# Kernel optimization log

Measured on AMD Instinct MI355X. Metric: run time of the kernel, lower is better.

The kernel has to match this reference:

```python
import jax, jax.numpy as jnp
import numpy as np

N_HEADS = 8

def setup_inputs() -> dict:
    key = jax.random.key(0)
    ks = jax.random.split(key, 12)
    B, S2, C, H, W = 2, 2048, 1280, 256, 256
    s = 0.02  # weight init scale
    return {
        'hidden_states': jax.random.normal(ks[0], (B, S2, C), dtype=jnp.float32),
        'src_mask': (jax.random.uniform(ks[1], (B, 1, H, W)) > 0.5).astype(jnp.float32),
        'attn_wq': jax.random.normal(ks[2], (C, C), dtype=jnp.float32) * s,
        'attn_wk': jax.random.normal(ks[3], (C, C), dtype=jnp.float32) * s,
        'attn_wv': jax.random.normal(ks[4], (C, C), dtype=jnp.float32) * s,
        'out_w': jax.random.normal(ks[5], (C, C), dtype=jnp.float32) * s,
        'out_b': jnp.zeros((C,), dtype=jnp.float32),
        'proc_wq': jax.random.normal(ks[6], (C, C), dtype=jnp.float32) * s,
        'proc_wk': jax.random.normal(ks[7], (C, C), dtype=jnp.float32) * s,
        'proc_wv': jax.random.normal(ks[8], (C, C), dtype=jnp.float32) * s,
        'ww': jax.random.normal(ks[9], (C + 1, 1), dtype=jnp.float32) * s,
        'wb': jnp.zeros((1,), dtype=jnp.float32),
    }


def reference(hidden_states, src_mask, attn_wq, attn_wk, attn_wv, out_w, out_b,
              proc_wq, proc_wk, proc_wv, ww, wb):
    B, S2, C = hidden_states.shape
    S = S2 // 2  # condition_flag=False: sequence is two images concatenated
    _, _, H, W = src_mask.shape
    r = int(np.sqrt((H * W) / S))  # nearest-neighbor downsample ratio
    # F.interpolate(mode='nearest') with exact integer ratio == strided slice
    m = src_mask[:, 0, ::r, ::r].reshape(B, S, 1)          # [B, S, 1]
    mask = jnp.concatenate([m, m], axis=1)                 # [B, 2S, 1]
    # sigmoid gate blending the two query projections
    gate_in = jnp.concatenate([hidden_states, mask], axis=-1)  # [B, 2S, C+1]
    w = jax.nn.sigmoid(gate_in @ ww + wb)                  # [B, 2S, 1]
    query = (hidden_states @ attn_wq) * w + (hidden_states @ proc_wq) * (1.0 - w)
    # keys/values: first half through attn's projections, second half through processor's
    e1, e2 = hidden_states[:, :S], hidden_states[:, S:]
    key = jnp.concatenate([e1 @ attn_wk, e2 @ proc_wk], axis=1)
    value = jnp.concatenate([e1 @ attn_wv, e2 @ proc_wv], axis=1)
    d = C // N_HEADS
    def split_heads(x):
        return x.reshape(B, S2, N_HEADS, d).transpose(0, 2, 1, 3)  # [B, H, S2, d]
    qh, kh, vh = split_heads(query), split_heads(key), split_heads(value)
    scale = float(1.0 / np.sqrt(d))
    scores = jnp.einsum('bhqd,bhkd->bhqk', qh, kh) * scale
    probs = jax.nn.softmax(scores, axis=-1)
    out = jnp.einsum('bhqk,bhkd->bhqd', probs, vh)
    out = out.transpose(0, 2, 1, 3).reshape(B, S2, C)
    out = out @ out_w + out_b
    # residual connection, rescale_output_factor == 1
    return out + hidden_states
```

## Files before the change

### kernel.cpp

```cpp
#include <hip/hip_runtime.h>

typedef unsigned short u16;
typedef u16 u16x4 __attribute__((ext_vector_type(4)));
typedef u16 u16x8 __attribute__((ext_vector_type(8)));
typedef __bf16 bf16x8 __attribute__((ext_vector_type(8)));
typedef float f32x4 __attribute__((ext_vector_type(4)));
typedef unsigned u32x4 __attribute__((ext_vector_type(4)));

#define DEVI __device__ __forceinline__

#if __has_builtin(__builtin_amdgcn_exp2f)
#define EXP2F __builtin_amdgcn_exp2f
#else
#define EXP2F exp2f
#endif

DEVI u16 f2b(float f) {
  unsigned u = __builtin_bit_cast(unsigned, f);
  u += 0x7fffu + ((u >> 16) & 1u);
  return (u16)(u >> 16);
}

DEVI float b2f(u16 v) { return __builtin_bit_cast(float, (unsigned)v << 16); }

DEVI unsigned cvtpk_bf16(float lo, float hi) {
  unsigned r;
  asm("v_cvt_pk_bf16_f32 %0, %1, %2" : "=v"(r) : "v"(lo), "v"(hi));
  return r;
}

DEVI f32x4 mfma16(u16x8 a, u16x8 b, f32x4 c) {
  return __builtin_amdgcn_mfma_f32_16x16x32_bf16(
      __builtin_bit_cast(bf16x8, a), __builtin_bit_cast(bf16x8, b), c, 0, 0, 0);
}

DEVI void async_copy16(const u16* g, u16* l) {
  __builtin_amdgcn_global_load_lds(
      (__attribute__((address_space(1))) unsigned int*)(g),
      (__attribute__((address_space(3))) unsigned int*)(l), 16, 0, 0);
}

DEVI void fence_barrier() {
  asm volatile("" ::: "memory");
  __builtin_amdgcn_s_barrier();
  asm volatile("" ::: "memory");
}

__global__ void prep_kernel(const float* __restrict__ hs, const float* __restrict__ mask,
                            const float* __restrict__ ww, const float* __restrict__ wb,
                            u16* __restrict__ hsb, float* __restrict__ wgate) {
  int token = blockIdx.x;
  int tid = threadIdx.x;
  const float* row = hs + (size_t)token * 1280;
  u16* orow = hsb + (size_t)token * 1280;
  float acc = 0.f;
#pragma unroll
  for (int i = 0; i < 5; i++) {
    int c = i * 256 + tid;
    float v = row[c];
    orow[c] = f2b(v);
    acc += v * ww[c];
  }
#pragma unroll
  for (int off = 1; off < 64; off <<= 1) acc += __shfl_xor(acc, off);
  __shared__ float partial[4];
  int wid = tid >> 6;
  if ((tid & 63) == 0) partial[wid] = acc;
  __syncthreads();
  if (tid == 0) {
    float tot = partial[0] + partial[1] + partial[2] + partial[3];
    int b = token >> 11, t = token & 2047;
    int s = t & 1023;
    float mv = mask[b * 65536 + ((s >> 5) * 8) * 256 + (s & 31) * 8];
    float z = tot + mv * ww[1280] + wb[0];
    wgate[token] = 1.f / (1.f + __expf(-z));
  }
}

__global__ void wtrans_kernel(const float* w0, const float* w1, const float* w2,
                              const float* w3, const float* w4, const float* w5,
                              const float* w6, u16* __restrict__ out) {
  const float* src;
  switch (blockIdx.z) {
    case 0: src = w0; break; case 1: src = w1; break; case 2: src = w2; break;
    case 3: src = w3; break; case 4: src = w4; break; case 5: src = w5; break;
    default: src = w6; break;
  }
  u16* dst = out + (size_t)blockIdx.z * 1280 * 1280;
  __shared__ float tile[32][33];
  int tx = threadIdx.x & 31, ty = threadIdx.x >> 5;
  int k0 = blockIdx.x * 32, n0 = blockIdx.y * 32;
#pragma unroll
  for (int r = 0; r < 4; r++)
    tile[ty + r * 8][tx] = src[(size_t)(k0 + ty + r * 8) * 1280 + n0 + tx];
  __syncthreads();
#pragma unroll
  for (int r = 0; r < 4; r++)
    dst[(size_t)(n0 + ty + r * 8) * 1280 + k0 + tx] = f2b(tile[tx][ty + r * 8]);
}

__launch_bounds__(256, 4)
__global__ void gemm_qdual_kernel(const u16* __restrict__ A, const u16* __restrict__ Wt,
                                  const float* __restrict__ wgate, float qscale,
                                  u16* __restrict__ Qout) {
  const int K = 1280, N = 1280;
  const size_t WSZ = (size_t)1280 * 1280;
  __shared__ u16 As[2][128 * 32];
  __shared__ u16 Bs[2][64 * 32];
  __shared__ u16 Bs2[2][64 * 32];

  int tid = threadIdx.x;
  int wid = tid >> 6, lane = tid & 63;
  int q = lane & 15, jl = lane >> 4;
  int nb = blockIdx.x, mb = blockIdx.y, z = blockIdx.z;
  int m0 = mb * 128, n0 = nb * 128;

  const u16* B0 = Wt + 0 * WSZ;
  const u16* B1 = Wt + 4 * WSZ;

  f32x4 zero = {0.f, 0.f, 0.f, 0.f};
  f32x4 acc[4][4];
#pragma unroll
  for (int i = 0; i < 4; i++)
#pragma unroll
    for (int j = 0; j < 4; j++) acc[i][j] = zero;

  int wr = wid >> 1, wc = wid & 1;
  int brow = tid >> 2, bseg = tid & 3;
  int nrow = n0 + (z << 6) + brow;

#define QSTAGE(buf, kk)                                                           \
  do {                                                                            \
    int k0 = (kk) * 32;                                                           \
    _Pragma("unroll") for (int i = 0; i < 2; i++) {                               \
      int slot = i * 256 + tid;                                                   \
      int row = slot >> 2, seg = slot & 3;                                        \
      async_copy16(A + (size_t)(m0 + row) * K + k0 + seg * 8,                     \
                   As[buf] + (size_t)(i * 256 + wid * 64) * 8);                   \
    }                                                                             \
    async_copy16(B0 + (size_t)nrow * K + k0 + bseg * 8, Bs[buf] + (size_t)tid * 8);   \
    async_copy16(B1 + (size_t)nrow * K + k0 + bseg * 8, Bs2[buf] + (size_t)tid * 8);  \
  } while (0)

  QSTAGE(0, 0);
  for (int kk = 0; kk < 40; kk++) {
    int cur = kk & 1;
    if (kk < 39) {
      QSTAGE(cur ^ 1, kk + 1);
      asm volatile("s_waitcnt vmcnt(4)" ::: "memory");
    } else {
      asm volatile("s_waitcnt vmcnt(0)" ::: "memory");
    }
    fence_barrier();

    u16x8 af[4];
#pragma unroll
    for (int mi = 0; mi < 4; mi++)
      af[mi] = *(const u16x8*)(As[cur] + (wr * 64 + mi * 16 + q) * 32 + jl * 8);
#pragma unroll
    for (int ni = 0; ni < 2; ni++) {
      u16x8 bf0 = *(const u16x8*)(Bs[cur] + (wc * 32 + ni * 16 + q) * 32 + jl * 8);
      u16x8 bf1 = *(const u16x8*)(Bs2[cur] + (wc * 32 + ni * 16 + q) * 32 + jl * 8);
#pragma unroll
      for (int mi = 0; mi < 4; mi++) {
        acc[mi][ni] = mfma16(af[mi], bf0, acc[mi][ni]);
        acc[mi][2 + ni] = mfma16(af[mi], bf1, acc[mi][2 + ni]);
      }
    }
    fence_barrier();
  }
#undef QSTAGE

#pragma unroll
  for (int mi = 0; mi < 4; mi++)
#pragma unroll
    for (int r = 0; r < 4; r++) {
      int row = m0 + wr * 64 + mi * 16 + (jl << 2) + r;
      float w = wgate[row];
#pragma unroll
      for (int ni = 0; ni < 2; ni++) {
        int col = n0 + (z << 6) + wc * 32 + ni * 16 + q;
        float v = (w * acc[mi][ni][r] + (1.f - w) * acc[mi][2 + ni][r]) * qscale;
        Qout[(size_t)row * N + col] = f2b(v);
      }
    }
}

__launch_bounds__(256, 4)
__global__ void gemm_kv_kernel(const u16* __restrict__ A, const u16* __restrict__ Wt,
                               u16* __restrict__ Kout, u16* __restrict__ VTout) {
  const int K = 1280, N = 1280;
  const size_t WSZ = (size_t)1280 * 1280;
  __shared__ u16 As[2][128 * 32];
  __shared__ u16 Bs[2][64 * 32];
  __shared__ u16 Bs2[2][64 * 32];

  int tid = threadIdx.x;
  int wid = tid >> 6, lane = tid & 63;
  int q = lane & 15, jl = lane >> 4;
  int nb = blockIdx.x, mb = blockIdx.y;
  bool isV = (blockIdx.z == 1);
  int m0 = mb * 128, n0 = nb * 128;
  bool first = ((m0 & 2047) < 1024);

  const u16* B0 = isV ? (first ? Wt + 2 * WSZ : Wt + 6 * WSZ)
                      : (first ? Wt + 1 * WSZ : Wt + 5 * WSZ);

  f32x4 zero = {0.f, 0.f, 0.f, 0.f};
  f32x4 acc[4][4];
#pragma unroll
  for (int i = 0; i < 4; i++)
#pragma unroll
    for (int j = 0; j < 4; j++) acc[i][j] = zero;

  int wr = wid >> 1, wc = wid & 1;
  int brow = tid >> 2, bseg = tid & 3;

#define KVSTAGE(buf, kk)                                                          \
  do {                                                                            \
    int k0 = (kk) * 32;                                                           \
    _Pragma("unroll") for (int i = 0; i < 2; i++) {                               \
      int slot = i * 256 + tid;                                                   \
      int row = slot >> 2, seg = slot & 3;                                        \
      async_copy16(A + (size_t)(m0 + row) * K + k0 + seg * 8,                     \
                   As[buf] + (size_t)(i * 256 + wid * 64) * 8);                   \
    }                                                                             \
    async_copy16(B0 + (size_t)(n0 + brow) * K + k0 + bseg * 8, Bs[buf] + (size_t)tid * 8);       \
    async_copy16(B0 + (size_t)(n0 + 64 + brow) * K + k0 + bseg * 8, Bs2[buf] + (size_t)tid * 8); \
  } while (0)

  KVSTAGE(0, 0);
  for (int kk = 0; kk < 40; kk++) {
    int cur = kk & 1;
    if (kk < 39) {
      KVSTAGE(cur ^ 1, kk + 1);
      asm volatile("s_waitcnt vmcnt(4)" ::: "memory");
    } else {
      asm volatile("s_waitcnt vmcnt(0)" ::: "memory");
    }
    fence_barrier();

    u16x8 af[4];
#pragma unroll
    for (int mi = 0; mi < 4; mi++)
      af[mi] = *(const u16x8*)(As[cur] + (wr * 64 + mi * 16 + q) * 32 + jl * 8);
    const u16* Bsel = wc ? Bs2[cur] : Bs[cur];
    u16x8 bfr[4];
#pragma unroll
    for (int ni = 0; ni < 4; ni++)
      bfr[ni] = *(const u16x8*)(Bsel + (ni * 16 + q) * 32 + jl * 8);
#pragma unroll
    for (int mi = 0; mi < 4; mi++)
#pragma unroll
      for (int ni = 0; ni < 4; ni++)
        acc[mi][ni] = mfma16(af[mi], bfr[ni], acc[mi][ni]);
    fence_barrier();
  }
#undef KVSTAGE

  if (!isV) {
#pragma unroll
    for (int mi = 0; mi < 4; mi++)
#pragma unroll
      for (int ni = 0; ni < 4; ni++)
#pragma unroll
        for (int r = 0; r < 4; r++) {
          int row = m0 + wr * 64 + mi * 16 + (jl << 2) + r;
          int col = n0 + wc * 64 + ni * 16 + q;
          Kout[(size_t)row * N + col] = f2b(acc[mi][ni][r]);
        }
  } else {
#pragma unroll
    for (int mi = 0; mi < 4; mi++)
#pragma unroll
      for (int ni = 0; ni < 4; ni++) {
        int row0 = m0 + wr * 64 + mi * 16 + (jl << 2);
        int col = n0 + wc * 64 + ni * 16 + q;
        int b = row0 >> 11, s = row0 & 2047;
        int h = col / 160, c_in = col - h * 160;
        u16x4 v = {f2b(acc[mi][ni][0]), f2b(acc[mi][ni][1]),
                   f2b(acc[mi][ni][2]), f2b(acc[mi][ni][3])};
        *(u16x4*)(VTout + ((size_t)(b * 8 + h) * 160 + c_in) * 2048 + s) = v;
      }
  }
}

template <int SPLIT>
__launch_bounds__(512)
__global__ void flash_kernel(const u16* __restrict__ Q, const u16* __restrict__ Kg,
                             const u16* __restrict__ VTg, u16* __restrict__ O,
                             u16* __restrict__ Opart, float* __restrict__ MLbuf) {
  const int C = 1280;
  int bid = blockIdx.x;
  int qb = bid & 15, h = (bid >> 4) & 7, b = bid >> 7;
  int sp = (SPLIT > 1) ? (int)blockIdx.y : 0;
  int tid = threadIdx.x, wid = tid >> 6, lane = tid & 63;
  int q = lane & 15, jl = lane >> 4;

  const int NT = 32 / SPLIT;
  const int t0 = sp * NT;

  const size_t baseQ = ((size_t)(b * 2048 + qb * 128)) * C + h * 160;
  const size_t baseK = ((size_t)(b * 2048)) * C + h * 160;
  const size_t baseVT = (size_t)(b * 8 + h) * 160 * 2048;

  __shared__ u16 Ks[64 * 160];
  __shared__ u16 Vts[160 * 64];

  const bool isK = (wid < 4);
  int sw = wid & 3;
  const u16* sbase;
  u16* sdst;
  size_t sadv;
  unsigned soff[5];
  if (isK) {
    sbase = Kg + baseK + (size_t)(t0 * 64) * C;
    sdst = Ks;
    sadv = (size_t)64 * C;
#pragma unroll
    for (int j = 0; j < 5; j++) {
      int s = (sw + 4 * j) * 64 + lane;
      int r = s / 20, cp = s - r * 20;
      int c = cp ^ ((r >> 1) & 3);
      soff[j] = (unsigned)(r * C + c * 8);
    }
  } else {
    sbase = VTg + baseVT + t0 * 64;
    sdst = Vts;
    sadv = 64;
#pragma unroll
    for (int j = 0; j < 5; j++) {
      int gc = (sw + 4 * j) * 64 + lane;
      int c = gc >> 3, jj = gc & 7;
      soff[j] = (unsigned)(c * 2048 + ((jj ^ (c & 7)) << 3));
    }
  }

#define STAGE5()                                                   \
  do {                                                             \
    _Pragma("unroll") for (int j = 0; j < 5; j++)                  \
        async_copy16(sbase + soff[j], sdst + (sw + 4 * j) * 512);  \
  } while (0)

  const int kro = ((jl ^ ((q >> 1) & 3)) << 3);

  const int addr0 = (q + 16 * ((jl * 2 + 0) & 3)) << 2;
  const int addr1 = (q + 16 * ((jl * 2 + 1) & 3)) << 2;
  const bool hihalf = (lane >= 32);

  u16x8 qf[5];
  {
    const u16* qrow = Q + baseQ + (size_t)(wid * 16 + q) * C;
#pragma unroll
    for (int ks = 0; ks < 5; ks++)
      qf[ks] = *(const u16x8*)(qrow + ks * 32 + jl * 8);
  }

  f32x4 zero = {0.f, 0.f, 0.f, 0.f};
  f32x4 oacc[10];
#pragma unroll
  for (int i = 0; i < 10; i++) oacc[i] = zero;
  float mrow = -1e30f, lrow = 0.f;

  STAGE5();

  for (int kti = 0; kti < NT; kti++) {
    bool last = (kti == NT - 1);
    if (isK) { asm volatile("s_waitcnt vmcnt(0)" ::: "memory"); }
    fence_barrier();

    f32x4 sc[4];
#pragma unroll
    for (int ct = 0; ct < 4; ct++) {
      f32x4 a = zero;
#pragma unroll
      for (int ks = 0; ks < 5; ks++) {
        u16x8 kf = *(const u16x8*)(&Ks[(ct * 16 + q) * 160 + ks * 32 + kro]);
        a = mfma16(kf, qf[ks], a);
      }
      sc[ct] = a;
    }

    fence_barrier();
    if (isK && !last) { sbase += sadv; STAGE5(); }

    float m = sc[0][0];
#pragma unroll
    for (int ct = 0; ct < 4; ct++)
#pragma unroll
      for (int r = 0; r < 4; r++) m = fmaxf(m, sc[ct][r]);
    m = fmaxf(m, __shfl_xor(m, 16));
    m = fmaxf(m, __shfl_xor(m, 32));

    if (__any(m > mrow + 8.f)) {
      float mnew = fmaxf(mrow, m);
      float alpha = EXP2F(mrow - mnew);
      mrow = mnew;
      float rs = 0.f;
#pragma unroll
      for (int ct = 0; ct < 4; ct++)
#pragma unroll
        for (int r = 0; r < 4; r++) {
          float p = EXP2F(sc[ct][r] - mnew);
          sc[ct][r] = p;
          rs += p;
        }
      lrow = lrow * alpha + rs;
#pragma unroll
      for (int ci = 0; ci < 10; ci++) oacc[ci] *= alpha;
    } else {
      float rs = 0.f;
#pragma unroll
      for (int ct = 0; ct < 4; ct++)
#pragma unroll
        for (int r = 0; r < 4; r++) {
          float p = EXP2F(sc[ct][r] - mrow);
          sc[ct][r] = p;
          rs += p;
        }
      lrow += rs;
    }

    unsigned pk0[4], pk1[4];
#pragma unroll
    for (int ct = 0; ct < 4; ct++) {
      pk0[ct] = cvtpk_bf16(sc[ct][0], sc[ct][1]);
      pk1[ct] = cvtpk_bf16(sc[ct][2], sc[ct][3]);
    }

    if (!isK) { asm volatile("s_waitcnt vmcnt(0)" ::: "memory"); }
    fence_barrier();

#pragma unroll
    for (int kt2 = 0; kt2 < 2; kt2++) {
      const int cA = kt2 * 2, cB = kt2 * 2 + 1;
      int a0 = __builtin_amdgcn_ds_bpermute(addr0, (int)pk0[cA]);
      int a1 = __builtin_amdgcn_ds_bpermute(addr0, (int)pk1[cA]);
      int a2 = __builtin_amdgcn_ds_bpermute(addr1, (int)pk0[cA]);
      int a3 = __builtin_amdgcn_ds_bpermute(addr1, (int)pk1[cA]);
      int b0 = __builtin_amdgcn_ds_bpermute(addr0, (int)pk0[cB]);
      int b1 = __builtin_amdgcn_ds_bpermute(addr0, (int)pk1[cB]);
      int b2 = __builtin_amdgcn_ds_bpermute(addr1, (int)pk0[cB]);
      int b3 = __builtin_amdgcn_ds_bpermute(addr1, (int)pk1[cB]);
      u32x4 d;
      d[0] = (unsigned)(hihalf ? b0 : a0);
      d[1] = (unsigned)(hihalf ? b1 : a1);
      d[2] = (unsigned)(hihalf ? b2 : a2);
      d[3] = (unsigned)(hihalf ? b3 : a3);
      u16x8 pf = __builtin_bit_cast(u16x8, d);
#pragma unroll
      for (int ci = 0; ci < 10; ci++) {
        int c = ci * 16 + q;
        int jj = kt2 * 4 + jl;
        u16x8 vf = *(const u16x8*)(&Vts[c * 64 + ((jj ^ (c & 7)) << 3)]);
        oacc[ci] = mfma16(vf, pf, oacc[ci]);
      }
    }

    fence_barrier();
    if (!isK && !last) { sbase += sadv; STAGE5(); }
  }
#undef STAGE5

  lrow += __shfl_xor(lrow, 16);
  lrow += __shfl_xor(lrow, 32);
  float linv = 1.f / lrow;

  int qrow = qb * 128 + wid * 16 + q;
  if constexpr (SPLIT > 1) {
    size_t g0 = (size_t)sp * 4096 + (size_t)b * 2048 + qrow;
#pragma unroll
    for (int ci = 0; ci < 10; ci++) {
      int col = h * 160 + ci * 16 + (jl << 2);
      u16x4 v = {f2b(oacc[ci][0] * linv), f2b(oacc[ci][1] * linv),
                 f2b(oacc[ci][2] * linv), f2b(oacc[ci][3] * linv)};
      *(u16x4*)(Opart + g0 * 1280 + col) = v;
    }
    if (lane < 16) {
      size_t mi = (g0 * 8 + h) * 2;
      MLbuf[mi] = mrow;
      MLbuf[mi + 1] = lrow;
    }
  } else {
#pragma unroll
    for (int ci = 0; ci < 10; ci++) {
      int col = h * 160 + ci * 16 + (jl << 2);
      u16x4 v = {f2b(oacc[ci][0] * linv), f2b(oacc[ci][1] * linv),
                 f2b(oacc[ci][2] * linv), f2b(oacc[ci][3] * linv)};
      *(u16x4*)(O + ((size_t)(b * 2048) + qrow) * C + col) = v;
    }
  }
}

__global__ void combine_kernel(const u16* __restrict__ Opart, const float* __restrict__ MLbuf,
                               u16* __restrict__ O) {
  int idx = blockIdx.x * 256 + threadIdx.x;
  int token = idx / 160;
  int h = (idx - token * 160) / 20;
  size_t i0 = ((size_t)token * 8 + h) * 2;
  const size_t MLP = (size_t)4096 * 16;
  float m0 = MLbuf[i0], l0 = MLbuf[i0 + 1];
  float m1 = MLbuf[i0 + MLP], l1 = MLbuf[i0 + MLP + 1];
  float m = fmaxf(m0, m1);
  float w0 = EXP2F(m0 - m) * l0, w1 = EXP2F(m1 - m) * l1;
  float inv = 1.f / (w0 + w1);
  w0 *= inv; w1 *= inv;
  const size_t OPP = (size_t)655360;
  u16x8 a = *(const u16x8*)(Opart + (size_t)idx * 8);
  u16x8 c = *(const u16x8*)(Opart + (OPP + idx) * 8);
  u16x8 o;
#pragma unroll
  for (int j = 0; j < 8; j++)
    o[j] = f2b(b2f(a[j]) * w0 + b2f(c[j]) * w1);
  *(u16x8*)(O + (size_t)idx * 8) = o;
}

__launch_bounds__(256, 4)
__global__ void gemm_out_kernel(const u16* __restrict__ A, const u16* __restrict__ Bt,
                                float* __restrict__ Cf, const float* __restrict__ bias,
                                const float* __restrict__ resid) {
  const int K = 1280, N = 1280;
  __shared__ u16 As[2][128 * 32];
  __shared__ u16 Bs[2][128 * 32];

  int tid = threadIdx.x;
  int wid = tid >> 6, lane = tid & 63;
  int nb = blockIdx.x, mb = blockIdx.y;
  int m0 = mb * 128, n0 = nb * 128;

  f32x4 zero = {0.f, 0.f, 0.f, 0.f};
  f32x4 acc[4][4];
#pragma unroll
  for (int i = 0; i < 4; i++)
#pragma unroll
    for (int j = 0; j < 4; j++) acc[i][j] = zero;

  int wr = wid >> 1, wc = wid & 1;

#define OSTAGE(buf, kk)                                                           \
  do {                                                                            \
    int k0 = (kk) * 32;                                                           \
    _Pragma("unroll") for (int i = 0; i < 2; i++) {                               \
      int slot = i * 256 + tid;                                                   \
      int row = slot >> 2, seg = slot & 3;                                        \
      async_copy16(A + (size_t)(m0 + row) * K + k0 + seg * 8,                     \
                   As[buf] + (size_t)(i * 256 + wid * 64) * 8);                   \
      async_copy16(Bt + (size_t)(n0 + row) * K + k0 + seg * 8,                    \
                   Bs[buf] + (size_t)(i * 256 + wid * 64) * 8);                   \
    }                                                                             \
  } while (0)

  OSTAGE(0, 0);
  for (int kk = 0; kk < 40; kk++) {
    int cur = kk & 1;
    if (kk < 39) {
      OSTAGE(cur ^ 1, kk + 1);
      asm volatile("s_waitcnt vmcnt(4)" ::: "memory");
    } else {
      asm volatile("s_waitcnt vmcnt(0)" ::: "memory");
    }
    fence_barrier();

    u16x8 af[4], bfr[4];
#pragma unroll
    for (int mi = 0; mi < 4; mi++)
      af[mi] = *(const u16x8*)(As[cur] + (wr * 64 + mi * 16 + (lane & 15)) * 32 + (lane >> 4) * 8);
#pragma unroll
    for (int ni = 0; ni < 4; ni++)
      bfr[ni] = *(const u16x8*)(Bs[cur] + (wc * 64 + ni * 16 + (lane & 15)) * 32 + (lane >> 4) * 8);
#pragma unroll
    for (int mi = 0; mi < 4; mi++)
#pragma unroll
      for (int ni = 0; ni < 4; ni++)
        acc[mi][ni] = mfma16(af[mi], bfr[ni], acc[mi][ni]);
    fence_barrier();
  }
#undef OSTAGE

#pragma unroll
  for (int mi = 0; mi < 4; mi++)
#pragma unroll
    for (int ni = 0; ni < 4; ni++)
#pragma unroll
      for (int r = 0; r < 4; r++) {
        int row = m0 + wr * 64 + mi * 16 + ((lane >> 4) << 2) + r;
        int col = n0 + wc * 64 + ni * 16 + (lane & 15);
        Cf[(size_t)row * N + col] = acc[mi][ni][r] + bias[col] + resid[(size_t)row * N + col];
      }
}

extern "C" void kernel_launch(void* const* d_in, const int* in_sizes, int n_in,
                              void* d_out, int out_size, void* d_ws, size_t ws_size,
                              hipStream_t stream) {
  const float* hs      = (const float*)d_in[0];
  const float* mask    = (const float*)d_in[1];
  const float* attn_wq = (const float*)d_in[2];
  const float* attn_wk = (const float*)d_in[3];
  const float* attn_wv = (const float*)d_in[4];
  const float* out_w   = (const float*)d_in[5];
  const float* out_b   = (const float*)d_in[6];
  const float* proc_wq = (const float*)d_in[7];
  const float* proc_wk = (const float*)d_in[8];
  const float* proc_wv = (const float*)d_in[9];
  const float* ww      = (const float*)d_in[10];
  const float* wb      = (const float*)d_in[11];
  float* out = (float*)d_out;

  char* ws = (char*)d_ws;
  const size_t TOK = (size_t)4096 * 1280;
  u16* hsb = (u16*)(ws);
  u16* Qb  = (u16*)(ws + 2 * TOK);
  u16* Kb  = (u16*)(ws + 4 * TOK);
  u16* VTb = (u16*)(ws + 6 * TOK);
  u16* AOb = (u16*)(ws + 8 * TOK);
  u16* Wt  = (u16*)(ws + 10 * TOK);
  float* wgate = (float*)(ws + 10 * TOK + (size_t)7 * 1280 * 1280 * 2);
  char* extra = ws + 10 * TOK + (size_t)7 * 1280 * 1280 * 2 + 16384;
  u16* Opart = (u16*)extra;
  float* MLbuf = (float*)(extra + (size_t)2 * 4096 * 1280 * 2);
  size_t need = (size_t)(extra - ws) + (size_t)2 * 4096 * 1280 * 2 + (size_t)2 * 4096 * 8 * 8;

  prep_kernel<<<4096, 256, 0, stream>>>(hs, mask, ww, wb, hsb, wgate);
  wtrans_kernel<<<dim3(40, 40, 7), 256, 0, stream>>>(attn_wq, attn_wk, attn_wv, out_w,
                                                     proc_wq, proc_wk, proc_wv, Wt);
  const size_t WSZ = (size_t)1280 * 1280;
  const float qscale = 0.11405505533858971f;
  gemm_qdual_kernel<<<dim3(10, 32, 2), 256, 0, stream>>>(hsb, Wt, wgate, qscale, Qb);
  gemm_kv_kernel<<<dim3(10, 32, 2), 256, 0, stream>>>(hsb, Wt, Kb, VTb);

  if (ws_size >= need) {
    flash_kernel<2><<<dim3(256, 2), 512, 0, stream>>>(Qb, Kb, VTb, nullptr, Opart, MLbuf);
    combine_kernel<<<2560, 256, 0, stream>>>(Opart, MLbuf, AOb);
  } else {
    flash_kernel<1><<<dim3(256, 1), 512, 0, stream>>>(Qb, Kb, VTb, AOb, nullptr, nullptr);
  }
  gemm_out_kernel<<<dim3(10, 32), 256, 0, stream>>>(AOb, Wt + 3 * WSZ, out, out_b, hs);
}
```

Measured before the change: 224.9 us.

## Process two 16-row query tiles per wave in flash attention

Each wave now computes attention for 32 query rows instead of 16, sharing every K and V shared-memory fragment across two independent MFMA accumulator sets. The block covers 256 query rows and the grid is halved. The aim is to cut LDS reads and barrier/staging overhead per unit of MFMA work. In exchange, per-thread registers roughly double, and the smaller grid may underfill the GPU and lower occupancy.

```diff
diff --git a/kernel.cpp b/kernel.cpp
--- a/kernel.cpp
+++ b/kernel.cpp
@@ -292,7 +292,7 @@
                              u16* __restrict__ Opart, float* __restrict__ MLbuf) {
   const int C = 1280;
   int bid = blockIdx.x;
-  int qb = bid & 15, h = (bid >> 4) & 7, b = bid >> 7;
+  int qb = bid & 7, h = (bid >> 3) & 7, b = bid >> 6;
   int sp = (SPLIT > 1) ? (int)blockIdx.y : 0;
   int tid = threadIdx.x, wid = tid >> 6, lane = tid & 63;
   int q = lane & 15, jl = lane >> 4;
@@ -300,7 +300,7 @@
   const int NT = 32 / SPLIT;
   const int t0 = sp * NT;
 
-  const size_t baseQ = ((size_t)(b * 2048 + qb * 128)) * C + h * 160;
+  const size_t baseQ = ((size_t)(b * 2048 + qb * 256)) * C + h * 160;
   const size_t baseK = ((size_t)(b * 2048)) * C + h * 160;
   const size_t baseVT = (size_t)(b * 8 + h) * 160 * 2048;
 
@@ -348,19 +348,23 @@
   const int addr1 = (q + 16 * ((jl * 2 + 1) & 3)) << 2;
   const bool hihalf = (lane >= 32);
 
-  u16x8 qf[5];
+  u16x8 qfA[5], qfB[5];
   {
-    const u16* qrow = Q + baseQ + (size_t)(wid * 16 + q) * C;
-#pragma unroll
-    for (int ks = 0; ks < 5; ks++)
-      qf[ks] = *(const u16x8*)(qrow + ks * 32 + jl * 8);
+    const u16* qrowA = Q + baseQ + (size_t)(wid * 32 + q) * C;
+    const u16* qrowB = qrowA + (size_t)16 * C;
+#pragma unroll
+    for (int ks = 0; ks < 5; ks++) {
+      qfA[ks] = *(const u16x8*)(qrowA + ks * 32 + jl * 8);
+      qfB[ks] = *(const u16x8*)(qrowB + ks * 32 + jl * 8);
+    }
   }
 
   f32x4 zero = {0.f, 0.f, 0.f, 0.f};
-  f32x4 oacc[10];
-#pragma unroll
-  for (int i = 0; i < 10; i++) oacc[i] = zero;
-  float mrow = -1e30f, lrow = 0.f;
+  f32x4 oaccA[10], oaccB[10];
+#pragma unroll
+  for (int i = 0; i < 10; i++) { oaccA[i] = zero; oaccB[i] = zero; }
+  float mrowA = -1e30f, lrowA = 0.f;
+  float mrowB = -1e30f, lrowB = 0.f;
 
   STAGE5();
 
@@ -369,63 +373,75 @@
     if (isK) { asm volatile("s_waitcnt vmcnt(0)" ::: "memory"); }
     fence_barrier();
 
-    f32x4 sc[4];
+    f32x4 scA[4], scB[4];
 #pragma unroll
     for (int ct = 0; ct < 4; ct++) {
-      f32x4 a = zero;
+      f32x4 aA = zero, aB = zero;
 #pragma unroll
       for (int ks = 0; ks < 5; ks++) {
         u16x8 kf = *(const u16x8*)(&Ks[(ct * 16 + q) * 160 + ks * 32 + kro]);
-        a = mfma16(kf, qf[ks], a);
+        aA = mfma16(kf, qfA[ks], aA);
+        aB = mfma16(kf, qfB[ks], aB);
       }
-      sc[ct] = a;
+      scA[ct] = aA;
+      scB[ct] = aB;
     }
 
     fence_barrier();
     if (isK && !last) { sbase += sadv; STAGE5(); }
 
-    float m = sc[0][0];
+    float mA = scA[0][0], mB = scB[0][0];
 #pragma unroll
     for (int ct = 0; ct < 4; ct++)
 #pragma unroll
-      for (int r = 0; r < 4; r++) m = fmaxf(m, sc[ct][r]);
-    m = fmaxf(m, __shfl_xor(m, 16));
-    m = fmaxf(m, __shfl_xor(m, 32));
-
-    if (__any(m > mrow + 8.f)) {
-      float mnew = fmaxf(mrow, m);
-      float alpha = EXP2F(mrow - mnew);
-      mrow = mnew;
-      float rs = 0.f;
+      for (int r = 0; r < 4; r++) {
+        mA = fmaxf(mA, scA[ct][r]);
+        mB = fmaxf(mB, scB[ct][r]);
+      }
+    mA = fmaxf(mA, __shfl_xor(mA, 16)); mA = fmaxf(mA, __shfl_xor(mA, 32));
+    mB = fmaxf(mB, __shfl_xor(mB, 16)); mB = fmaxf(mB, __shfl_xor(mB, 32));
+
+    bool need = (mA > mrowA + 8.f) || (mB > mrowB + 8.f);
+    if (__any(need)) {
+      float mnA = fmaxf(mrowA, mA), mnB = fmaxf(mrowB, mB);
+      float alA = EXP2F(mrowA - mnA), alB = EXP2F(mrowB - mnB);
+      mrowA = mnA; mrowB = mnB;
+      float rsA = 0.f, rsB = 0.f;
 #pragma unroll
       for (int ct = 0; ct < 4; ct++)
 #pragma unroll
         for (int r = 0; r < 4; r++) {
-          float p = EXP2F(sc[ct][r] - mnew);
-          sc[ct][r] = p;
-          rs += p;
+          float pA = EXP2F(scA[ct][r] - mnA);
+          float pB = EXP2F(scB[ct][r] - mnB);
+          scA[ct][r] = pA; scB[ct][r] = pB;
+          rsA += pA; rsB += pB;
         }
-      lrow = lrow * alpha + rs;
-#pragma unroll
-      for (int ci = 0; ci < 10; ci++) oacc[ci] *= alpha;
+      lrowA = lrowA * alA + rsA;
+      lrowB = lrowB * alB + rsB;
+#pragma unroll
+      for (int ci = 0; ci < 10; ci++) { oaccA[ci] *= alA; oaccB[ci] *= alB; }
     } else {
-      float rs = 0.f;
+      float rsA = 0.f, rsB = 0.f;
 #pragma unroll
       for (int ct = 0; ct < 4; ct++)
 #pragma unroll
         for (int r = 0; r < 4; r++) {
-          float p = EXP2F(sc[ct][r] - mrow);
-          sc[ct][r] = p;
-          rs += p;
+          float pA = EXP2F(scA[ct][r] - mrowA);
+          float pB = EXP2F(scB[ct][r] - mrowB);
+          scA[ct][r] = pA; scB[ct][r] = pB;
+          rsA += pA; rsB += pB;
         }
-      lrow += rs;
-    }
-
-    unsigned pk0[4], pk1[4];
+      lrowA += rsA;
+      lrowB += rsB;
+    }
+
+    unsigned pkA0[4], pkA1[4], pkB0[4], pkB1[4];
 #pragma unroll
     for (int ct = 0; ct < 4; ct++) {
-      pk0[ct] = cvtpk_bf16(sc[ct][0], sc[ct][1]);
-      pk1[ct] = cvtpk_bf16(sc[ct][2], sc[ct][3]);
+      pkA0[ct] = cvtpk_bf16(scA[ct][0], scA[ct][1]);
+      pkA1[ct] = cvtpk_bf16(scA[ct][2], scA[ct][3]);
+      pkB0[ct] = cvtpk_bf16(scB[ct][0], scB[ct][1]);
+      pkB1[ct] = cvtpk_bf16(scB[ct][2], scB[ct][3]);
     }
 
     if (!isK) { asm volatile("s_waitcnt vmcnt(0)" ::: "memory"); }
@@ -434,26 +450,41 @@
 #pragma unroll
     for (int kt2 = 0; kt2 < 2; kt2++) {
       const int cA = kt2 * 2, cB = kt2 * 2 + 1;
-      int a0 = __builtin_amdgcn_ds_bpermute(addr0, (int)pk0[cA]);
-      int a1 = __builtin_amdgcn_ds_bpermute(addr0, (int)pk1[cA]);
-      int a2 = __builtin_amdgcn_ds_bpermute(addr1, (int)pk0[cA]);
-      int a3 = __builtin_amdgcn_ds_bpermute(addr1, (int)pk1[cA]);
-      int b0 = __builtin_amdgcn_ds_bpermute(addr0, (int)pk0[cB]);
-      int b1 = __builtin_amdgcn_ds_bpermute(addr0, (int)pk1[cB]);
-      int b2 = __builtin_amdgcn_ds_bpermute(addr1, (int)pk0[cB]);
-      int b3 = __builtin_amdgcn_ds_bpermute(addr1, (int)pk1[cB]);
-      u32x4 d;
-      d[0] = (unsigned)(hihalf ? b0 : a0);
-      d[1] = (unsigned)(hihalf ? b1 : a1);
-      d[2] = (unsigned)(hihalf ? b2 : a2);
-      d[3] = (unsigned)(hihalf ? b3 : a3);
-      u16x8 pf = __builtin_bit_cast(u16x8, d);
+      int a0 = __builtin_amdgcn_ds_bpermute(addr0, (int)pkA0[cA]);
+      int a1 = __builtin_amdgcn_ds_bpermute(addr0, (int)pkA1[cA]);
+      int a2 = __builtin_amdgcn_ds_bpermute(addr1, (int)pkA0[cA]);
+      int a3 = __builtin_amdgcn_ds_bpermute(addr1, (int)pkA1[cA]);
+      int b0 = __builtin_amdgcn_ds_bpermute(addr0, (int)pkA0[cB]);
+      int b1 = __builtin_amdgcn_ds_bpermute(addr0, (int)pkA1[cB]);
+      int b2 = __builtin_amdgcn_ds_bpermute(addr1, (int)pkA0[cB]);
+      int b3 = __builtin_amdgcn_ds_bpermute(addr1, (int)pkA1[cB]);
+      u32x4 dA;
+      dA[0] = (unsigned)(hihalf ? b0 : a0);
+      dA[1] = (unsigned)(hihalf ? b1 : a1);
+      dA[2] = (unsigned)(hihalf ? b2 : a2);
+      dA[3] = (unsigned)(hihalf ? b3 : a3);
+      u16x8 pfA = __builtin_bit_cast(u16x8, dA);
+      a0 = __builtin_amdgcn_ds_bpermute(addr0, (int)pkB0[cA]);
+      a1 = __builtin_amdgcn_ds_bpermute(addr0, (int)pkB1[cA]);
+      a2 = __builtin_amdgcn_ds_bpermute(addr1, (int)pkB0[cA]);
+      a3 = __builtin_amdgcn_ds_bpermute(addr1, (int)pkB1[cA]);
+      b0 = __builtin_amdgcn_ds_bpermute(addr0, (int)pkB0[cB]);
+      b1 = __builtin_amdgcn_ds_bpermute(addr0, (int)pkB1[cB]);
+      b2 = __builtin_amdgcn_ds_bpermute(addr1, (int)pkB0[cB]);
+      b3 = __builtin_amdgcn_ds_bpermute(addr1, (int)pkB1[cB]);
+      u32x4 dB;
+      dB[0] = (unsigned)(hihalf ? b0 : a0);
+      dB[1] = (unsigned)(hihalf ? b1 : a1);
+      dB[2] = (unsigned)(hihalf ? b2 : a2);
+      dB[3] = (unsigned)(hihalf ? b3 : a3);
+      u16x8 pfB = __builtin_bit_cast(u16x8, dB);
 #pragma unroll
       for (int ci = 0; ci < 10; ci++) {
         int c = ci * 16 + q;
         int jj = kt2 * 4 + jl;
         u16x8 vf = *(const u16x8*)(&Vts[c * 64 + ((jj ^ (c & 7)) << 3)]);
-        oacc[ci] = mfma16(vf, pf, oacc[ci]);
+        oaccA[ci] = mfma16(vf, pfA, oaccA[ci]);
+        oaccB[ci] = mfma16(vf, pfB, oaccB[ci]);
       }
     }
 
@@ -462,32 +493,41 @@
   }
 #undef STAGE5
 
-  lrow += __shfl_xor(lrow, 16);
-  lrow += __shfl_xor(lrow, 32);
-  float linv = 1.f / lrow;
-
-  int qrow = qb * 128 + wid * 16 + q;
+  lrowA += __shfl_xor(lrowA, 16); lrowA += __shfl_xor(lrowA, 32);
+  lrowB += __shfl_xor(lrowB, 16); lrowB += __shfl_xor(lrowB, 32);
+  float linvA = 1.f / lrowA, linvB = 1.f / lrowB;
+
+  int qrowA = qb * 256 + wid * 32 + q;
+  int qrowB = qrowA + 16;
   if constexpr (SPLIT > 1) {
-    size_t g0 = (size_t)sp * 4096 + (size_t)b * 2048 + qrow;
+    size_t g0A = (size_t)sp * 4096 + (size_t)b * 2048 + qrowA;
+    size_t g0B = g0A + 16;
 #pragma unroll
     for (int ci = 0; ci < 10; ci++) {
       int col = h * 160 + ci * 16 + (jl << 2);
-      u16x4 v = {f2b(oacc[ci][0] * linv), f2b(oacc[ci][1] * linv),
-                 f2b(oacc[ci][2] * linv), f2b(oacc[ci][3] * linv)};
-      *(u16x4*)(Opart + g0 * 1280 + col) = v;
+      u16x4 vA = {f2b(oaccA[ci][0] * linvA), f2b(oaccA[ci][1] * linvA),
+                  f2b(oaccA[ci][2] * linvA), f2b(oaccA[ci][3] * linvA)};
+      u16x4 vB = {f2b(oaccB[ci][0] * linvB), f2b(oaccB[ci][1] * linvB),
+                  f2b(oaccB[ci][2] * linvB), f2b(oaccB[ci][3] * linvB)};
+      *(u16x4*)(Opart + g0A * 1280 + col) = vA;
+      *(u16x4*)(Opart + g0B * 1280 + col) = vB;
     }
     if (lane < 16) {
-      size_t mi = (g0 * 8 + h) * 2;
-      MLbuf[mi] = mrow;
-      MLbuf[mi + 1] = lrow;
+      size_t miA = (g0A * 8 + h) * 2;
+      size_t miB = (g0B * 8 + h) * 2;
+      MLbuf[miA] = mrowA; MLbuf[miA + 1] = lrowA;
+      MLbuf[miB] = mrowB; MLbuf[miB + 1] = lrowB;
     }
   } else {
 #pragma unroll
     for (int ci = 0; ci < 10; ci++) {
       int col = h * 160 + ci * 16 + (jl << 2);
-      u16x4 v = {f2b(oacc[ci][0] * linv), f2b(oacc[ci][1] * linv),
-                 f2b(oacc[ci][2] * linv), f2b(oacc[ci][3] * linv)};
-      *(u16x4*)(O + ((size_t)(b * 2048) + qrow) * C + col) = v;
+      u16x4 vA = {f2b(oaccA[ci][0] * linvA), f2b(oaccA[ci][1] * linvA),
+                  f2b(oaccA[ci][2] * linvA), f2b(oaccA[ci][3] * linvA)};
+      u16x4 vB = {f2b(oaccB[ci][0] * linvB), f2b(oaccB[ci][1] * linvB),
+                  f2b(oaccB[ci][2] * linvB), f2b(oaccB[ci][3] * linvB)};
+      *(u16x4*)(O + ((size_t)(b * 2048) + qrowA) * C + col) = vA;
+      *(u16x4*)(O + ((size_t)(b * 2048) + qrowB) * C + col) = vB;
     }
   }
 }
@@ -629,10 +669,10 @@
   gemm_kv_kernel<<<dim3(10, 32, 2), 256, 0, stream>>>(hsb, Wt, Kb, VTb);
 
   if (ws_size >= need) {
-    flash_kernel<2><<<dim3(256, 2), 512, 0, stream>>>(Qb, Kb, VTb, nullptr, Opart, MLbuf);
+    flash_kernel<2><<<dim3(128, 2), 512, 0, stream>>>(Qb, Kb, VTb, nullptr, Opart, MLbuf);
     combine_kernel<<<2560, 256, 0, stream>>>(Opart, MLbuf, AOb);
   } else {
-    flash_kernel<1><<<dim3(256, 1), 512, 0, stream>>>(Qb, Kb, VTb, AOb, nullptr, nullptr);
+    flash_kernel<1><<<dim3(128, 1), 512, 0, stream>>>(Qb, Kb, VTb, AOb, nullptr, nullptr);
   }
   gemm_out_kernel<<<dim3(10, 32), 256, 0, stream>>>(AOb, Wt + 3 * WSZ, out, out_b, hs);
 }
```

Measured after the change: 314.1 us. 1.4x slower.
